# Kernel tuning notes

Measured on AMD Instinct MI355X. Metric: run time of the kernel, lower is better.

Reference implementation:

```python
import jax, jax.numpy as jnp
import numpy as np

N_SRC0, N_DST0, N_DST1 = 100000, 20000, 4000
E0, E1 = 640000, 128000
IN_F, HID_F, OUT_F = 512, 512, 256


def _graph_conv(x_src, src, dst, W, b, n_src, n_dst):
    """DGL GraphConv, norm='both': D_out^{-1/2} A D_in^{-1/2} X W + b."""
    ones_e = jnp.ones(src.shape[0], x_src.dtype)
    out_deg = jnp.maximum(jax.ops.segment_sum(ones_e, src, num_segments=n_src), 1.0)
    in_deg = jnp.maximum(jax.ops.segment_sum(ones_e, dst, num_segments=n_dst), 1.0)
    h = x_src * (out_deg ** -0.5)[:, None]          # [n_src, F] pre-normalize
    agg = jax.ops.segment_sum(h[src], dst, num_segments=n_dst)  # gather -> scatter-add
    agg = agg * (in_deg ** -0.5)[:, None]           # [n_dst, F]
    return agg @ W + b


def setup_inputs() -> dict:
    key = jax.random.key(0)
    ks = jax.random.split(key, 8)
    x = jax.random.normal(ks[0], (N_SRC0, IN_F), jnp.float32)
    src0 = jax.random.randint(ks[1], (E0,), 0, N_SRC0)
    dst0 = jax.random.randint(ks[2], (E0,), 0, N_DST0)
    src1 = jax.random.randint(ks[3], (E1,), 0, N_DST0)
    dst1 = jax.random.randint(ks[4], (E1,), 0, N_DST1)
    W1 = jax.random.normal(ks[5], (IN_F, HID_F), jnp.float32) * (IN_F ** -0.5)
    b1 = jnp.zeros((HID_F,), jnp.float32)
    W2 = jax.random.normal(ks[6], (HID_F, OUT_F), jnp.float32) * (HID_F ** -0.5)
    b2 = jnp.zeros((OUT_F,), jnp.float32)
    return {"x": x, "src0": src0, "dst0": dst0, "src1": src1, "dst1": dst1,
            "W1": W1, "b1": b1, "W2": W2, "b2": b2,
            "n_src0": N_SRC0, "n_dst0": N_DST0, "n_dst1": N_DST1}


def reference(x, src0, dst0, src1, dst1, W1, b1, W2, b2, n_src0, n_dst0, n_dst1):
    h = jax.nn.relu(_graph_conv(x, src0, dst0, W1, b1, n_src0, n_dst0))
    out = jax.nn.relu(_graph_conv(h, src1, dst1, W2, b2, n_dst0, n_dst1))
    return out
```

## Files before the change

kernel.cpp:

```cpp
#include <hip/hip_runtime.h>

typedef unsigned short ushort_t;
typedef unsigned int uint_t;
typedef __attribute__((ext_vector_type(8))) short s8v;
typedef __attribute__((ext_vector_type(4))) float f4v;

#define NS0 100000
#define ND0 20000
#define ND1 4000
#define E0  640000
#define E1  128000
#define F   512
#define OF  256

__device__ __forceinline__ ushort_t f2b(float f) {
    uint_t u = __float_as_uint(f);
    uint_t r = (u + 0x7fffu + ((u >> 16) & 1u)) >> 16;
    return (ushort_t)r;
}
__device__ __forceinline__ float b2f_lo(uint_t u) { return __uint_as_float(u << 16); }
__device__ __forceinline__ float b2f_hi(uint_t u) { return __uint_as_float(u & 0xffff0000u); }

__global__ __launch_bounds__(256) void count_deg(const int* __restrict__ src0, const int* __restrict__ dst0,
                                                 const int* __restrict__ src1, const int* __restrict__ dst1,
                                                 int* __restrict__ cnt) {
    int i = blockIdx.x * 256 + threadIdx.x;
    int stride = gridDim.x * 256;
    for (int e = i; e < E0; e += stride) {
        atomicAdd(&cnt[src0[e]], 1);
        atomicAdd(&cnt[NS0 + dst0[e]], 1);
    }
    for (int e = i; e < E1; e += stride) {
        atomicAdd(&cnt[NS0 + ND0 + src1[e]], 1);
        atomicAdd(&cnt[NS0 + ND0 + ND0 + dst1[e]], 1);
    }
}

__global__ __launch_bounds__(256) void rsq_kernel(const int* __restrict__ cnt, float* __restrict__ rsq, int n) {
    int i = blockIdx.x * 256 + threadIdx.x;
    if (i < n) rsq[i] = rsqrtf(fmaxf((float)cnt[i], 1.0f));
}

__global__ __launch_bounds__(1024) void scan_excl(const int* __restrict__ cnt, int n,
                                                  int* __restrict__ off, int* __restrict__ cur) {
    __shared__ int wsum[16];
    __shared__ int wexc[16];
    __shared__ int tsum;
    __shared__ int carry;
    int lid = threadIdx.x;
    int lane = lid & 63;
    int w = lid >> 6;
    if (lid == 0) carry = 0;
    __syncthreads();
    for (int base = 0; base < n; base += 1024) {
        int i = base + lid;
        int v = (i < n) ? cnt[i] : 0;
        int s = v;
        #pragma unroll
        for (int d = 1; d < 64; d <<= 1) {
            int t = __shfl_up(s, d, 64);
            if (lane >= d) s += t;
        }
        if (lane == 63) wsum[w] = s;
        __syncthreads();
        if (w == 0 && lane < 16) {
            int ws = wsum[lane];
            int ss = ws;
            #pragma unroll
            for (int d = 1; d < 16; d <<= 1) {
                int t = __shfl_up(ss, d, 64);
                if (lane >= d) ss += t;
            }
            wexc[lane] = ss - ws;
            if (lane == 15) tsum = ss;
        }
        __syncthreads();
        int excl = carry + wexc[w] + s - v;
        if (i < n) { off[i] = excl; cur[i] = excl; }
        __syncthreads();
        if (lid == 0) carry += tsum;
        __syncthreads();
    }
}

__global__ __launch_bounds__(256) void fill_edges(const int* __restrict__ src0, const int* __restrict__ dst0,
                                                  const int* __restrict__ src1, const int* __restrict__ dst1,
                                                  int* __restrict__ cur0, int* __restrict__ cur1,
                                                  int* __restrict__ es0, int* __restrict__ es1) {
    int i = blockIdx.x * 256 + threadIdx.x;
    int stride = gridDim.x * 256;
    for (int e = i; e < E0; e += stride) {
        int d = dst0[e];
        int p = atomicAdd(&cur0[d], 1);
        es0[p] = src0[e];
    }
    for (int e = i; e < E1; e += stride) {
        int d = dst1[e];
        int p = atomicAdd(&cur1[d], 1);
        es1[p] = src1[e];
    }
}

__global__ __launch_bounds__(256) void conv_w(const float* __restrict__ W1, const float* __restrict__ W2,
                                              ushort_t* __restrict__ wt1, ushort_t* __restrict__ wt2) {
    int i = blockIdx.x * 256 + threadIdx.x;
    if (i < F * F) {
        int k = i >> 9, n = i & (F - 1);
        wt1[n * F + k] = f2b(W1[i]);
    } else if (i < F * F + F * OF) {
        int j = i - F * F;
        int k = j >> 8, n = j & (OF - 1);
        wt2[n * F + k] = f2b(W2[j]);
    }
}

__global__ __launch_bounds__(256) void conv_x(const float* __restrict__ x, const float* __restrict__ rsq_out0,
                                              ushort_t* __restrict__ xb) {
    int i = blockIdx.x * 256 + threadIdx.x;
    if (i >= NS0 * 128) return;
    int row = i >> 7;
    float4 v = ((const float4*)x)[i];
    float sc = rsq_out0[row];
    uint2 o;
    o.x = (uint_t)f2b(v.x * sc) | ((uint_t)f2b(v.y * sc) << 16);
    o.y = (uint_t)f2b(v.z * sc) | ((uint_t)f2b(v.w * sc) << 16);
    ((uint2*)xb)[i] = o;
}

__device__ __forceinline__ void add8(float* acc, uint4 u) {
    acc[0] += b2f_lo(u.x); acc[1] += b2f_hi(u.x);
    acc[2] += b2f_lo(u.y); acc[3] += b2f_hi(u.y);
    acc[4] += b2f_lo(u.z); acc[5] += b2f_hi(u.z);
    acc[6] += b2f_lo(u.w); acc[7] += b2f_hi(u.w);
}

__global__ __launch_bounds__(256) void agg_bf16(const ushort_t* __restrict__ X, const int* __restrict__ es,
                                                const int* __restrict__ off, const int* __restrict__ cnt,
                                                const float* __restrict__ rsq_in, ushort_t* __restrict__ out,
                                                int ndst) {
    int d = __builtin_amdgcn_readfirstlane(blockIdx.x * 4 + (threadIdx.x >> 6));
    if (d >= ndst) return;
    int lane = threadIdx.x & 63;
    int base = off[d], n = cnt[d];
    const uint4* Xv = (const uint4*)X;
    float acc[8] = {0.f, 0.f, 0.f, 0.f, 0.f, 0.f, 0.f, 0.f};
    int i = 0;
    for (; i + 4 <= n; i += 4) {
        int s0 = es[base + i];
        int s1 = es[base + i + 1];
        int s2 = es[base + i + 2];
        int s3 = es[base + i + 3];
        uint4 u0 = Xv[(size_t)s0 * 64 + lane];
        uint4 u1 = Xv[(size_t)s1 * 64 + lane];
        uint4 u2 = Xv[(size_t)s2 * 64 + lane];
        uint4 u3 = Xv[(size_t)s3 * 64 + lane];
        add8(acc, u0); add8(acc, u1); add8(acc, u2); add8(acc, u3);
    }
    for (; i < n; ++i) {
        int s = es[base + i];
        uint4 u = Xv[(size_t)s * 64 + lane];
        add8(acc, u);
    }
    float sc = rsq_in[d];
    uint4 o;
    o.x = (uint_t)f2b(acc[0] * sc) | ((uint_t)f2b(acc[1] * sc) << 16);
    o.y = (uint_t)f2b(acc[2] * sc) | ((uint_t)f2b(acc[3] * sc) << 16);
    o.z = (uint_t)f2b(acc[4] * sc) | ((uint_t)f2b(acc[5] * sc) << 16);
    o.w = (uint_t)f2b(acc[6] * sc) | ((uint_t)f2b(acc[7] * sc) << 16);
    ((uint4*)out)[(size_t)d * 64 + lane] = o;
}

__global__ __launch_bounds__(256) void agg_f32(const float* __restrict__ X, const float* __restrict__ rsq_out,
                                               const int* __restrict__ es, const int* __restrict__ off,
                                               const int* __restrict__ cnt, const float* __restrict__ rsq_in,
                                               ushort_t* __restrict__ out) {
    int d = blockIdx.x;
    int t = threadIdx.x;
    int base = off[d], n = cnt[d];
    float ax = 0.f, ay = 0.f;
    for (int i = 0; i < n; ++i) {
        int s = es[base + i];
        float2 v = ((const float2*)X)[(size_t)s * 256 + t];
        float sc = rsq_out[s];
        ax += v.x * sc;
        ay += v.y * sc;
    }
    float sc = rsq_in[d];
    ax *= sc; ay *= sc;
    ((uint_t*)out)[(size_t)d * 256 + t] = (uint_t)f2b(ax) | ((uint_t)f2b(ay) << 16);
}

template <typename OutT>
__global__ __launch_bounds__(256) void gemm_bias_relu(const ushort_t* __restrict__ A, const ushort_t* __restrict__ BT,
                                                      const float* __restrict__ bias, const float* __restrict__ rowScale,
                                                      OutT* __restrict__ C, int M, int N, int K) {
    __shared__ __align__(16) ushort_t As[64 * 72];
    __shared__ __align__(16) ushort_t Bs[64 * 72];
    int tid = threadIdx.x;
    int lane = tid & 63;
    int w = tid >> 6;
    int m16 = lane & 15, quad = lane >> 4;
    int r = tid >> 2;
    int cseg = (tid & 3) * 8;
    int rowA = blockIdx.x * 64 + r; if (rowA >= M) rowA = M - 1;
    int rowB = blockIdx.y * 64 + r;
    f4v acc[4] = {};
    for (int k0 = 0; k0 < K; k0 += 64) {
        *(uint4*)&As[r * 72 + cseg]      = *(const uint4*)(A + (size_t)rowA * K + k0 + cseg);
        *(uint4*)&As[r * 72 + cseg + 32] = *(const uint4*)(A + (size_t)rowA * K + k0 + cseg + 32);
        *(uint4*)&Bs[r * 72 + cseg]      = *(const uint4*)(BT + (size_t)rowB * K + k0 + cseg);
        *(uint4*)&Bs[r * 72 + cseg + 32] = *(const uint4*)(BT + (size_t)rowB * K + k0 + cseg + 32);
        __syncthreads();
        #pragma unroll
        for (int kc = 0; kc < 2; ++kc) {
            const int co = kc * 32 + quad * 8;
            s8v bf = *(const s8v*)&Bs[(w * 16 + m16) * 72 + co];
            s8v a0 = *(const s8v*)&As[(m16) * 72 + co];
            s8v a1 = *(const s8v*)&As[(16 + m16) * 72 + co];
            s8v a2 = *(const s8v*)&As[(32 + m16) * 72 + co];
            s8v a3 = *(const s8v*)&As[(48 + m16) * 72 + co];
            acc[0] = __builtin_amdgcn_mfma_f32_16x16x32_bf16(a0, bf, acc[0], 0, 0, 0);
            acc[1] = __builtin_amdgcn_mfma_f32_16x16x32_bf16(a1, bf, acc[1], 0, 0, 0);
            acc[2] = __builtin_amdgcn_mfma_f32_16x16x32_bf16(a2, bf, acc[2], 0, 0, 0);
            acc[3] = __builtin_amdgcn_mfma_f32_16x16x32_bf16(a3, bf, acc[3], 0, 0, 0);
        }
        __syncthreads();
    }
    int col = blockIdx.y * 64 + w * 16 + m16;
    float b = bias[col];
    #pragma unroll
    for (int mt = 0; mt < 4; ++mt) {
        #pragma unroll
        for (int rr = 0; rr < 4; ++rr) {
            int row = blockIdx.x * 64 + mt * 16 + quad * 4 + rr;
            if (row < M) {
                float v = acc[mt][rr] + b;
                v = fmaxf(v, 0.0f);
                if (rowScale) v *= rowScale[row];
                if (sizeof(OutT) == 2)
                    ((ushort_t*)C)[(size_t)row * N + col] = f2b(v);
                else
                    ((float*)C)[(size_t)row * N + col] = v;
            }
        }
    }
}

extern "C" void kernel_launch(void* const* d_in, const int* in_sizes, int n_in,
                              void* d_out, int out_size, void* d_ws, size_t ws_size,
                              hipStream_t stream) {
    (void)in_sizes; (void)n_in; (void)out_size;
    const float* x    = (const float*)d_in[0];
    const int*   src0 = (const int*)d_in[1];
    const int*   dst0 = (const int*)d_in[2];
    const int*   src1 = (const int*)d_in[3];
    const int*   dst1 = (const int*)d_in[4];
    const float* W1   = (const float*)d_in[5];
    const float* b1   = (const float*)d_in[6];
    const float* W2   = (const float*)d_in[7];
    const float* b2   = (const float*)d_in[8];
    float* out = (float*)d_out;

    char* p = (char*)d_ws;
    auto alloc = [&](size_t bytes) { char* q = p; p += (bytes + 255) & ~(size_t)255; return q; };
    const int NCNT = NS0 + ND0 + ND0 + ND1;
    int*      cnt  = (int*)alloc((size_t)NCNT * 4);
    float*    rsq  = (float*)alloc((size_t)NCNT * 4);
    int*      off0 = (int*)alloc((size_t)ND0 * 4);
    int*      cur0 = (int*)alloc((size_t)ND0 * 4);
    int*      off1 = (int*)alloc((size_t)ND1 * 4);
    int*      cur1 = (int*)alloc((size_t)ND1 * 4);
    int*      es0  = (int*)alloc((size_t)E0 * 4);
    int*      es1  = (int*)alloc((size_t)E1 * 4);
    ushort_t* wt1  = (ushort_t*)alloc((size_t)F * F * 2);
    ushort_t* wt2  = (ushort_t*)alloc((size_t)OF * F * 2);
    ushort_t* agg0 = (ushort_t*)alloc((size_t)ND0 * F * 2);
    ushort_t* h    = (ushort_t*)alloc((size_t)ND0 * F * 2);
    ushort_t* agg1 = (ushort_t*)alloc((size_t)ND1 * F * 2);
    size_t used = (size_t)(p - (char*)d_ws);
    bool use_xb = (ws_size >= used + (size_t)NS0 * F * 2 + 512);
    ushort_t* xb = use_xb ? (ushort_t*)alloc((size_t)NS0 * F * 2) : nullptr;

    const float* rsq_out0 = rsq;
    const float* rsq_in0  = rsq + NS0;
    const float* rsq_out1 = rsq + NS0 + ND0;
    const float* rsq_in1  = rsq + NS0 + ND0 + ND0;

    hipMemsetAsync(cnt, 0, (size_t)NCNT * 4, stream);
    count_deg<<<E0 / 256, 256, 0, stream>>>(src0, dst0, src1, dst1, cnt);
    rsq_kernel<<<(NCNT + 255) / 256, 256, 0, stream>>>(cnt, rsq, NCNT);
    scan_excl<<<1, 1024, 0, stream>>>(cnt + NS0, ND0, off0, cur0);
    scan_excl<<<1, 1024, 0, stream>>>(cnt + NS0 + ND0 + ND0, ND1, off1, cur1);
    fill_edges<<<E0 / 256, 256, 0, stream>>>(src0, dst0, src1, dst1, cur0, cur1, es0, es1);
    conv_w<<<(F * F + F * OF) / 256, 256, 0, stream>>>(W1, W2, wt1, wt2);

    if (use_xb) {
        conv_x<<<(NS0 * 128 + 255) / 256, 256, 0, stream>>>(x, rsq_out0, xb);
        agg_bf16<<<(ND0 + 3) / 4, 256, 0, stream>>>(xb, es0, off0, cnt + NS0, rsq_in0, agg0, ND0);
    } else {
        agg_f32<<<ND0, 256, 0, stream>>>(x, rsq_out0, es0, off0, cnt + NS0, rsq_in0, agg0);
    }

    gemm_bias_relu<ushort_t><<<dim3((ND0 + 63) / 64, F / 64), 256, 0, stream>>>(
        agg0, wt1, b1, rsq_out1, h, ND0, F, F);

    agg_bf16<<<(ND1 + 3) / 4, 256, 0, stream>>>(h, es1, off1, cnt + NS0 + ND0 + ND0, rsq_in1, agg1, ND1);

    gemm_bias_relu<float><<<dim3((ND1 + 63) / 64, OF / 64), 256, 0, stream>>>(
        agg1, wt2, b2, nullptr, out, ND1, OF, F);
}
```

Measured before the change: 608.8 us.

## Use 128x128 GEMM tiles with direct LDS loads, merge scans, deepen gather unroll

The GEMM moves from 64x64 to 128x128 block tiles, with each wave computing a 64x64 sub-tile. Tiles are loaded straight into LDS with global_load_lds, which raises data reuse per MFMA. The two serial exclusive scans become one two-block launch using per-thread chunked sums, removing a serial loop and one launch. The bf16 gather loop unrolls to 8 loads to keep more memory requests in flight. Risks: the unpadded LDS layout may cause bank conflicts, and the larger tiles give fewer blocks for the small second GEMM.

```diff
diff --git a/kernel.cpp b/kernel.cpp
--- a/kernel.cpp
+++ b/kernel.cpp
@@ -41,45 +41,40 @@
     if (i < n) rsq[i] = rsqrtf(fmaxf((float)cnt[i], 1.0f));
 }
 
-__global__ __launch_bounds__(1024) void scan_excl(const int* __restrict__ cnt, int n,
-                                                  int* __restrict__ off, int* __restrict__ cur) {
+__global__ __launch_bounds__(1024) void scan_both(const int* __restrict__ cnt0, int n0,
+                                                  int* __restrict__ off0, int* __restrict__ cur0,
+                                                  const int* __restrict__ cnt1, int n1,
+                                                  int* __restrict__ off1, int* __restrict__ cur1) {
+    const int* cnt = blockIdx.x ? cnt1 : cnt0;
+    int n = blockIdx.x ? n1 : n0;
+    int* off = blockIdx.x ? off1 : off0;
+    int* cur = blockIdx.x ? cur1 : cur0;
     __shared__ int wsum[16];
     __shared__ int wexc[16];
-    __shared__ int tsum;
-    __shared__ int carry;
-    int lid = threadIdx.x;
-    int lane = lid & 63;
-    int w = lid >> 6;
-    if (lid == 0) carry = 0;
+    int lid = threadIdx.x, lane = lid & 63, w = lid >> 6;
+    int ch = (n + 1023) >> 10;
+    int s0 = lid * ch;
+    int e0 = min(s0 + ch, n);
+    int sum = 0;
+    for (int i = s0; i < e0; ++i) sum += cnt[i];
+    int s = sum;
+    #pragma unroll
+    for (int d = 1; d < 64; d <<= 1) { int t = __shfl_up(s, d, 64); if (lane >= d) s += t; }
+    if (lane == 63) wsum[w] = s;
     __syncthreads();
-    for (int base = 0; base < n; base += 1024) {
-        int i = base + lid;
-        int v = (i < n) ? cnt[i] : 0;
-        int s = v;
-        #pragma unroll
-        for (int d = 1; d < 64; d <<= 1) {
-            int t = __shfl_up(s, d, 64);
-            if (lane >= d) s += t;
-        }
-        if (lane == 63) wsum[w] = s;
-        __syncthreads();
-        if (w == 0 && lane < 16) {
-            int ws = wsum[lane];
-            int ss = ws;
-            #pragma unroll
-            for (int d = 1; d < 16; d <<= 1) {
-                int t = __shfl_up(ss, d, 64);
-                if (lane >= d) ss += t;
-            }
-            wexc[lane] = ss - ws;
-            if (lane == 15) tsum = ss;
-        }
-        __syncthreads();
-        int excl = carry + wexc[w] + s - v;
-        if (i < n) { off[i] = excl; cur[i] = excl; }
-        __syncthreads();
-        if (lid == 0) carry += tsum;
-        __syncthreads();
+    if (w == 0 && lane < 16) {
+        int ws = wsum[lane];
+        int ss = ws;
+        #pragma unroll
+        for (int d = 1; d < 16; d <<= 1) { int t = __shfl_up(ss, d, 64); if (lane >= d) ss += t; }
+        wexc[lane] = ss - ws;
+    }
+    __syncthreads();
+    int run = wexc[w] + s - sum;
+    for (int i = s0; i < e0; ++i) {
+        int v = cnt[i];
+        off[i] = run; cur[i] = run;
+        run += v;
     }
 }
 
@@ -145,22 +140,19 @@
     const uint4* Xv = (const uint4*)X;
     float acc[8] = {0.f, 0.f, 0.f, 0.f, 0.f, 0.f, 0.f, 0.f};
     int i = 0;
-    for (; i + 4 <= n; i += 4) {
-        int s0 = es[base + i];
-        int s1 = es[base + i + 1];
-        int s2 = es[base + i + 2];
-        int s3 = es[base + i + 3];
-        uint4 u0 = Xv[(size_t)s0 * 64 + lane];
-        uint4 u1 = Xv[(size_t)s1 * 64 + lane];
-        uint4 u2 = Xv[(size_t)s2 * 64 + lane];
-        uint4 u3 = Xv[(size_t)s3 * 64 + lane];
-        add8(acc, u0); add8(acc, u1); add8(acc, u2); add8(acc, u3);
-    }
-    for (; i < n; ++i) {
-        int s = es[base + i];
-        uint4 u = Xv[(size_t)s * 64 + lane];
-        add8(acc, u);
-    }
+    for (; i + 8 <= n; i += 8) {
+        uint4 u[8];
+        #pragma unroll
+        for (int j = 0; j < 8; ++j) u[j] = Xv[(size_t)es[base + i + j] * 64 + lane];
+        #pragma unroll
+        for (int j = 0; j < 8; ++j) add8(acc, u[j]);
+    }
+    for (; i + 2 <= n; i += 2) {
+        uint4 u0 = Xv[(size_t)es[base + i] * 64 + lane];
+        uint4 u1 = Xv[(size_t)es[base + i + 1] * 64 + lane];
+        add8(acc, u0); add8(acc, u1);
+    }
+    if (i < n) add8(acc, Xv[(size_t)es[base + i] * 64 + lane]);
     float sc = rsq_in[d];
     uint4 o;
     o.x = (uint_t)f2b(acc[0] * sc) | ((uint_t)f2b(acc[1] * sc) << 16);
@@ -191,56 +183,71 @@
 }
 
 template <typename OutT>
-__global__ __launch_bounds__(256) void gemm_bias_relu(const ushort_t* __restrict__ A, const ushort_t* __restrict__ BT,
-                                                      const float* __restrict__ bias, const float* __restrict__ rowScale,
-                                                      OutT* __restrict__ C, int M, int N, int K) {
-    __shared__ __align__(16) ushort_t As[64 * 72];
-    __shared__ __align__(16) ushort_t Bs[64 * 72];
+__global__ __launch_bounds__(256) void gemm128(const ushort_t* __restrict__ A, const ushort_t* __restrict__ BT,
+                                               const float* __restrict__ bias, const float* __restrict__ rowScale,
+                                               OutT* __restrict__ C, int M, int N, int K) {
+    __shared__ __align__(16) ushort_t As[128 * 64];
+    __shared__ __align__(16) ushort_t Bs[128 * 64];
     int tid = threadIdx.x;
-    int lane = tid & 63;
-    int w = tid >> 6;
+    int lane = tid & 63, w = tid >> 6;
     int m16 = lane & 15, quad = lane >> 4;
-    int r = tid >> 2;
-    int cseg = (tid & 3) * 8;
-    int rowA = blockIdx.x * 64 + r; if (rowA >= M) rowA = M - 1;
-    int rowB = blockIdx.y * 64 + r;
-    f4v acc[4] = {};
+    int wm = w & 1, wn = w >> 1;
+    int bm = blockIdx.x * 128, bn = blockIdx.y * 128;
+    f4v acc[4][4] = {};
     for (int k0 = 0; k0 < K; k0 += 64) {
-        *(uint4*)&As[r * 72 + cseg]      = *(const uint4*)(A + (size_t)rowA * K + k0 + cseg);
-        *(uint4*)&As[r * 72 + cseg + 32] = *(const uint4*)(A + (size_t)rowA * K + k0 + cseg + 32);
-        *(uint4*)&Bs[r * 72 + cseg]      = *(const uint4*)(BT + (size_t)rowB * K + k0 + cseg);
-        *(uint4*)&Bs[r * 72 + cseg + 32] = *(const uint4*)(BT + (size_t)rowB * K + k0 + cseg + 32);
-        __syncthreads();
-        #pragma unroll
-        for (int kc = 0; kc < 2; ++kc) {
-            const int co = kc * 32 + quad * 8;
-            s8v bf = *(const s8v*)&Bs[(w * 16 + m16) * 72 + co];
-            s8v a0 = *(const s8v*)&As[(m16) * 72 + co];
-            s8v a1 = *(const s8v*)&As[(16 + m16) * 72 + co];
-            s8v a2 = *(const s8v*)&As[(32 + m16) * 72 + co];
-            s8v a3 = *(const s8v*)&As[(48 + m16) * 72 + co];
-            acc[0] = __builtin_amdgcn_mfma_f32_16x16x32_bf16(a0, bf, acc[0], 0, 0, 0);
-            acc[1] = __builtin_amdgcn_mfma_f32_16x16x32_bf16(a1, bf, acc[1], 0, 0, 0);
-            acc[2] = __builtin_amdgcn_mfma_f32_16x16x32_bf16(a2, bf, acc[2], 0, 0, 0);
-            acc[3] = __builtin_amdgcn_mfma_f32_16x16x32_bf16(a3, bf, acc[3], 0, 0, 0);
+        #pragma unroll
+        for (int i = 0; i < 4; ++i) {
+            int c = i * 256 + tid;
+            int row = c >> 3, seg = (c & 7) * 8;
+            int ra = bm + row; if (ra >= M) ra = M - 1;
+            __builtin_amdgcn_global_load_lds(
+                (const __attribute__((address_space(1))) uint_t*)(A + (size_t)ra * K + k0 + seg),
+                (__attribute__((address_space(3))) uint_t*)(As + (size_t)c * 8), 16, 0, 0);
+        }
+        #pragma unroll
+        for (int i = 0; i < 4; ++i) {
+            int c = i * 256 + tid;
+            int row = c >> 3, seg = (c & 7) * 8;
+            int rb = bn + row;
+            __builtin_amdgcn_global_load_lds(
+                (const __attribute__((address_space(1))) uint_t*)(BT + (size_t)rb * K + k0 + seg),
+                (__attribute__((address_space(3))) uint_t*)(Bs + (size_t)c * 8), 16, 0, 0);
         }
         __syncthreads();
-    }
-    int col = blockIdx.y * 64 + w * 16 + m16;
-    float b = bias[col];
+        #pragma unroll
+        for (int kc = 0; kc < 2; ++kc) {
+            int co = kc * 32 + quad * 8;
+            s8v af[4], bf[4];
+            #pragma unroll
+            for (int m = 0; m < 4; ++m)
+                af[m] = *(const s8v*)&As[(wm * 64 + m * 16 + m16) * 64 + co];
+            #pragma unroll
+            for (int nn = 0; nn < 4; ++nn)
+                bf[nn] = *(const s8v*)&Bs[(wn * 64 + nn * 16 + m16) * 64 + co];
+            #pragma unroll
+            for (int m = 0; m < 4; ++m)
+                #pragma unroll
+                for (int nn = 0; nn < 4; ++nn)
+                    acc[m][nn] = __builtin_amdgcn_mfma_f32_16x16x32_bf16(af[m], bf[nn], acc[m][nn], 0, 0, 0);
+        }
+        __syncthreads();
+    }
     #pragma unroll
-    for (int mt = 0; mt < 4; ++mt) {
+    for (int m = 0; m < 4; ++m) {
         #pragma unroll
         for (int rr = 0; rr < 4; ++rr) {
-            int row = blockIdx.x * 64 + mt * 16 + quad * 4 + rr;
+            int row = bm + wm * 64 + m * 16 + quad * 4 + rr;
             if (row < M) {
-                float v = acc[mt][rr] + b;
-                v = fmaxf(v, 0.0f);
-                if (rowScale) v *= rowScale[row];
-                if (sizeof(OutT) == 2)
-                    ((ushort_t*)C)[(size_t)row * N + col] = f2b(v);
-                else
-                    ((float*)C)[(size_t)row * N + col] = v;
+                float rs = rowScale ? rowScale[row] : 1.0f;
+                #pragma unroll
+                for (int nn = 0; nn < 4; ++nn) {
+                    int col = bn + wn * 64 + nn * 16 + m16;
+                    float v = fmaxf(acc[m][nn][rr] + bias[col], 0.0f) * rs;
+                    if (sizeof(OutT) == 2)
+                        ((ushort_t*)C)[(size_t)row * N + col] = f2b(v);
+                    else
+                        ((float*)C)[(size_t)row * N + col] = v;
+                }
             }
         }
     }
@@ -289,8 +296,8 @@
     hipMemsetAsync(cnt, 0, (size_t)NCNT * 4, stream);
     count_deg<<<E0 / 256, 256, 0, stream>>>(src0, dst0, src1, dst1, cnt);
     rsq_kernel<<<(NCNT + 255) / 256, 256, 0, stream>>>(cnt, rsq, NCNT);
-    scan_excl<<<1, 1024, 0, stream>>>(cnt + NS0, ND0, off0, cur0);
-    scan_excl<<<1, 1024, 0, stream>>>(cnt + NS0 + ND0 + ND0, ND1, off1, cur1);
+    scan_both<<<2, 1024, 0, stream>>>(cnt + NS0, ND0, off0, cur0,
+                                      cnt + NS0 + ND0 + ND0, ND1, off1, cur1);
     fill_edges<<<E0 / 256, 256, 0, stream>>>(src0, dst0, src1, dst1, cur0, cur1, es0, es1);
     conv_w<<<(F * F + F * OF) / 256, 256, 0, stream>>>(W1, W2, wt1, wt2);
 
@@ -301,11 +308,11 @@
         agg_f32<<<ND0, 256, 0, stream>>>(x, rsq_out0, es0, off0, cnt + NS0, rsq_in0, agg0);
     }
 
-    gemm_bias_relu<ushort_t><<<dim3((ND0 + 63) / 64, F / 64), 256, 0, stream>>>(
+    gemm128<ushort_t><<<dim3((ND0 + 127) / 128, F / 128), 256, 0, stream>>>(
         agg0, wt1, b1, rsq_out1, h, ND0, F, F);
 
     agg_bf16<<<(ND1 + 3) / 4, 256, 0, stream>>>(h, es1, off1, cnt + NS0 + ND0 + ND0, rsq_in1, agg1, ND1);
 
-    gemm_bias_relu<float><<<dim3((ND1 + 63) / 64, OF / 64), 256, 0, stream>>>(
+    gemm128<float><<<dim3((ND1 + 127) / 128, OF / 128), 256, 0, stream>>>(
         agg1, wt2, b2, nullptr, out, ND1, OF, F);
 }
```

Result: no change. 608.2 us (-0.1%).
